# Kernel optimization log

Measured on AMD Instinct MI355X. Metric: run time of the kernel, lower is better.

Reference implementation:

```python
import jax, jax.numpy as jnp
import numpy as np

D_MODEL = 2048
NUM_HEADS = 32
NUM_KV_GROUPS = 8
D_K = D_MODEL // NUM_HEADS  # 64
KV_DIM = D_K * NUM_KV_GROUPS  # 512
B, S = 2, 2048


def setup_inputs() -> dict:
    key = jax.random.key(0)
    ks = jax.random.split(key, 9)
    sd = 1.0 / np.sqrt(D_MODEL).astype(np.float32)
    return {
        "x": jax.random.normal(ks[0], (B, S, D_MODEL), jnp.float32),
        "wq": jax.random.normal(ks[1], (D_MODEL, D_MODEL), jnp.float32) * sd,
        "bq": jnp.zeros((D_MODEL,), jnp.float32),
        "wk": jax.random.normal(ks[2], (D_MODEL, KV_DIM), jnp.float32) * sd,
        "bk": jnp.zeros((KV_DIM,), jnp.float32),
        "wv": jax.random.normal(ks[3], (D_MODEL, KV_DIM), jnp.float32) * sd,
        "bv": jnp.zeros((KV_DIM,), jnp.float32),
        "wo": jax.random.normal(ks[4], (D_MODEL, D_MODEL), jnp.float32) * sd,
        "bo": jnp.zeros((D_MODEL,), jnp.float32),
    }


def reference(x, wq, bq, wk, bk, wv, bv, wo, bo):
    b, s, _ = x.shape
    # projections (torch Linear = x @ W^T + b; weights here stored as (in,out))
    Q = (x @ wq + bq).reshape(b, s, NUM_HEADS, D_K).transpose(0, 2, 1, 3)       # [B,H,S,dk]
    K = (x @ wk + bk).reshape(b, s, NUM_KV_GROUPS, D_K).transpose(0, 2, 1, 3)   # [B,G,S,dk]
    V = (x @ wv + bv).reshape(b, s, NUM_KV_GROUPS, D_K).transpose(0, 2, 1, 3)   # [B,G,S,dk]
    kv_repeat = NUM_HEADS // NUM_KV_GROUPS
    K_rep = jnp.repeat(K, kv_repeat, axis=1)  # [B,H,S,dk]
    V_rep = jnp.repeat(V, kv_repeat, axis=1)  # [B,H,S,dk]
    scale = 1.0 / jnp.sqrt(jnp.asarray(D_K, x.dtype))
    attn_scores = jnp.einsum("bhqd,bhkd->bhqk", Q, K_rep) * scale
    attn_weights = jax.nn.softmax(attn_scores, axis=-1)                          # [B,H,S,S]
    context = jnp.einsum("bhqk,bhkd->bhqd", attn_weights, V_rep)
    context = context.transpose(0, 2, 1, 3).reshape(b, s, D_MODEL)
    return context @ wo + bo
```

## Files before the change

kernel.cpp:

```cpp
#include <hip/hip_runtime.h>
#include <hip/hip_bf16.h>

typedef __bf16 v8bf16 __attribute__((ext_vector_type(8)));
typedef __bf16 bf16x4 __attribute__((ext_vector_type(4)));
typedef float  f32x4  __attribute__((ext_vector_type(4)));

#define D_MODEL 2048
#define S_LEN   2048
#define NHEADS  32
#define NGROUPS 8
#define DK      64
#define NTOK    4096
#define NQKV    3072
#define QSCALE  0.18033688011112042f

__device__ __forceinline__ void lds_load16(const void* g, void* l) {
  __builtin_amdgcn_global_load_lds(
      (__attribute__((address_space(1))) unsigned int*)g,
      (__attribute__((address_space(3))) unsigned int*)l, 16, 0, 0);
}

__device__ __forceinline__ int sw64(int row, int col) {
  return row * 64 + (col ^ ((row & 7) << 3));
}

__global__ __launch_bounds__(256)
void cvt_f32_bf16(const float* __restrict__ in, __bf16* __restrict__ out, int n) {
  int i = (blockIdx.x * 256 + threadIdx.x) * 4;
  if (i >= n) return;
  float4 v = *(const float4*)(in + i);
  bf16x4 o = { (__bf16)v.x, (__bf16)v.y, (__bf16)v.z, (__bf16)v.w };
  *(bf16x4*)(out + i) = o;
}

__global__ __launch_bounds__(256)
void transpose_cvt(const float* __restrict__ in, __bf16* __restrict__ out, int R, int C) {
  __shared__ float tile[32][33];
  int tx = threadIdx.x, ty = threadIdx.y;
  int c0 = blockIdx.x * 32, r0 = blockIdx.y * 32;
#pragma unroll
  for (int j = 0; j < 4; j++)
    tile[ty + 8 * j][tx] = in[(size_t)(r0 + ty + 8 * j) * C + c0 + tx];
  __syncthreads();
#pragma unroll
  for (int j = 0; j < 4; j++)
    out[(size_t)(c0 + ty + 8 * j) * R + r0 + tx] = (__bf16)tile[tx][ty + 8 * j];
}

__global__ __launch_bounds__(256)
void transpose_bf16(const __bf16* __restrict__ in, __bf16* __restrict__ out,
                    int R, int C, int ldin, int ldout) {
  __shared__ __bf16 tile[32][33];
  int tx = threadIdx.x, ty = threadIdx.y;
  int c0 = blockIdx.x * 32, r0 = blockIdx.y * 32;
#pragma unroll
  for (int j = 0; j < 4; j++)
    tile[ty + 8 * j][tx] = in[(size_t)(r0 + ty + 8 * j) * ldin + c0 + tx];
  __syncthreads();
#pragma unroll
  for (int j = 0; j < 4; j++)
    out[(size_t)(c0 + ty + 8 * j) * ldout + r0 + tx] = tile[tx][ty + 8 * j];
}

template <int MODE, int BN>
__global__ __launch_bounds__(512, 1)
void gemm_big(const __bf16* __restrict__ A, const __bf16* __restrict__ BT,
              const float* __restrict__ b0, const float* __restrict__ b1,
              const float* __restrict__ b2,
              __bf16* __restrict__ Cb, float* __restrict__ Cf,
              int M, int N, int K) {
  constexpr int FN = BN / 64;
  __shared__ __bf16 Alds[2 * 256 * 64];
  __shared__ __bf16 Blds[2 * BN * 64];
  const int t = threadIdx.x;
  const int lane = t & 63, w = t >> 6;
  const int lr = lane & 15, lg = lane >> 4;
  const int wm = w >> 2, wn = w & 3;
  const int cpx = gridDim.x >> 3;
  const int swz = (blockIdx.x & 7) * cpx + (blockIdx.x >> 3);
  const int nbx = N / BN;
  const int m0 = (swz / nbx) * 256, n0 = (swz % nbx) * BN;
  const int scol = (((t & 7) ^ ((t >> 3) & 7)) << 3);

  const __bf16* ap = A + (size_t)(m0 + (t >> 3)) * K + scol;
  const __bf16* bp = BT + (size_t)(n0 + (t >> 3)) * K + scol;

  auto stage = [&](int buf) {
    __bf16* ad = Alds + buf * 16384 + t * 8;
    __bf16* bd = Blds + buf * BN * 64 + t * 8;
#pragma unroll
    for (int i = 0; i < 4; i++) lds_load16(ap + (size_t)i * 64 * K, ad + i * 4096);
#pragma unroll
    for (int i = 0; i < FN; i++) lds_load16(bp + (size_t)i * 64 * K, bd + i * 4096);
    ap += 64; bp += 64;
  };

  const f32x4 fz = {0.f, 0.f, 0.f, 0.f};
  f32x4 acc[8][FN];
#pragma unroll
  for (int fm = 0; fm < 8; fm++)
#pragma unroll
    for (int fn = 0; fn < FN; fn++) acc[fm][fn] = fz;

  auto compute = [&](int buf) {
    const __bf16* Ab = Alds + buf * 16384;
    const __bf16* Bb = Blds + buf * BN * 64;
#pragma unroll
    for (int ks = 0; ks < 2; ks++) {
      v8bf16 bfr[FN];
#pragma unroll
      for (int fn = 0; fn < FN; fn++)
        bfr[fn] = *(const v8bf16*)&Bb[sw64(wn * (BN / 4) + fn * 16 + lr, ks * 32 + lg * 8)];
      __builtin_amdgcn_s_setprio(1);
#pragma unroll
      for (int fm = 0; fm < 8; fm++) {
        v8bf16 af = *(const v8bf16*)&Ab[sw64(wm * 128 + fm * 16 + lr, ks * 32 + lg * 8)];
#pragma unroll
        for (int fn = 0; fn < FN; fn++)
          acc[fm][fn] = __builtin_amdgcn_mfma_f32_16x16x32_bf16(af, bfr[fn], acc[fm][fn], 0, 0, 0);
      }
      __builtin_amdgcn_s_setprio(0);
    }
  };

  stage(0);
  stage(1);
  for (int kt = 0; kt < 32; kt++) {
    if (kt < 31) {
      if constexpr (FN == 3) asm volatile("s_waitcnt vmcnt(7)" ::: "memory");
      else                   asm volatile("s_waitcnt vmcnt(6)" ::: "memory");
    } else {
      asm volatile("s_waitcnt vmcnt(0)" ::: "memory");
    }
    __builtin_amdgcn_s_barrier();
    __builtin_amdgcn_sched_barrier(0);
    compute(kt & 1);
    if (kt < 30) {
      __builtin_amdgcn_sched_barrier(0);
      __builtin_amdgcn_s_barrier();
      __builtin_amdgcn_sched_barrier(0);
      stage(kt & 1);
    }
  }

#pragma unroll
  for (int fn = 0; fn < FN; fn++) {
    int col = n0 + wn * (BN / 4) + fn * 16 + lr;
    float bias, scale = 1.0f;
    if (MODE == 0) {
      if (col < 2048)      { bias = b0[col];        scale = QSCALE; }
      else if (col < 2560) { bias = b1[col - 2048]; }
      else                 { bias = b2[col - 2560]; }
    } else {
      bias = b0[col];
    }
#pragma unroll
    for (int fm = 0; fm < 8; fm++)
#pragma unroll
      for (int r = 0; r < 4; r++) {
        int row = m0 + wm * 128 + fm * 16 + lg * 4 + r;
        float v = acc[fm][fn][r] + bias;
        if (MODE == 0) Cb[(size_t)row * N + col] = (__bf16)(v * scale);
        else           Cf[(size_t)row * N + col] = v;
      }
  }
}

__global__ __launch_bounds__(512, 2)
void attn_kernel(const __bf16* __restrict__ QKV, const __bf16* __restrict__ VT,
                 __bf16* __restrict__ ctx) {
  __shared__ __bf16 smem[26624];
  const int t = threadIdx.x;
  const int lane = t & 63, w = t >> 6;
  const int lr = lane & 15, lg = lane >> 4;
  const int flat = blockIdx.y * 8 + blockIdx.x;
  const int swz = (flat & 7) * 64 + (flat >> 3);
  const int qt = swz & 7, bh = swz >> 3;
  const int b = bh >> 5, h = bh & 31, g = h >> 2;
  const int q0 = qt * 256;
  const int scol = (((t & 7) ^ ((t >> 3) & 7)) << 3);

  v8bf16 qa[2][2];
#pragma unroll
  for (int mi = 0; mi < 2; mi++)
#pragma unroll
    for (int dk2 = 0; dk2 < 2; dk2++)
      qa[mi][dk2] = *(const v8bf16*)(QKV +
          (size_t)(b * S_LEN + q0 + w * 32 + mi * 16 + lr) * NQKV + h * DK + dk2 * 32 + lg * 8);

  const __bf16* kp = QKV + (size_t)(b * S_LEN + (t >> 3)) * NQKV + D_MODEL + g * DK + scol;
  const __bf16* vp = VT + (size_t)(g * DK + (t >> 3)) * NTOK + b * S_LEN + scol;

  lds_load16(kp, smem + t * 8);
  lds_load16(vp, smem + 4096 + t * 8);
  __syncthreads();

  const int kloff0 = lr * 64 + ((lg * 8) ^ ((lr & 7) << 3));
  const int kloff1 = lr * 64 + ((32 + lg * 8) ^ ((lr & 7) << 3));
  __bf16* Pw = smem + 16384 + w * 1280;

  const __bf16 one1 = (__bf16)1.0f;
  const v8bf16 ones = { one1, one1, one1, one1, one1, one1, one1, one1 };
  const f32x4 fz = {0.f, 0.f, 0.f, 0.f};
  f32x4 o[2][4], o_sum[2];
  o_sum[0] = fz; o_sum[1] = fz;
#pragma unroll
  for (int mi = 0; mi < 2; mi++)
#pragma unroll
    for (int nd = 0; nd < 4; nd++) o[mi][nd] = fz;

#pragma unroll 2
  for (int kt = 0; kt < 32; kt++) {
    if (kt < 31) {
      __bf16* nb = smem + ((kt & 1) ^ 1) * 8192;
      lds_load16(kp + (size_t)64 * NQKV, nb + t * 8);
      lds_load16(vp + 64, nb + 4096 + t * 8);
      kp += (size_t)64 * NQKV;
      vp += 64;
    }
    const __bf16* Kb = smem + (kt & 1) * 8192;
    const __bf16* k0 = Kb + kloff0;
    const __bf16* k1 = Kb + kloff1;

    f32x4 st[4][2];
#pragma unroll
    for (int ni = 0; ni < 4; ni++) { st[ni][0] = fz; st[ni][1] = fz; }
    __builtin_amdgcn_s_setprio(1);
#pragma unroll
    for (int ni = 0; ni < 4; ni++) {
      v8bf16 kb = *(const v8bf16*)(k0 + ni * 1024);
      st[ni][0] = __builtin_amdgcn_mfma_f32_16x16x32_bf16(kb, qa[0][0], st[ni][0], 0, 0, 0);
      st[ni][1] = __builtin_amdgcn_mfma_f32_16x16x32_bf16(kb, qa[1][0], st[ni][1], 0, 0, 0);
    }
#pragma unroll
    for (int ni = 0; ni < 4; ni++) {
      v8bf16 kb = *(const v8bf16*)(k1 + ni * 1024);
      st[ni][0] = __builtin_amdgcn_mfma_f32_16x16x32_bf16(kb, qa[0][1], st[ni][0], 0, 0, 0);
      st[ni][1] = __builtin_amdgcn_mfma_f32_16x16x32_bf16(kb, qa[1][1], st[ni][1], 0, 0, 0);
    }
    __builtin_amdgcn_s_setprio(0);

#pragma unroll
    for (int ks = 0; ks < 2; ks++) {
      const __bf16* vbase = (ks ? k1 : k0) + 4096;
#pragma unroll
      for (int mi = 0; mi < 2; mi++)
#pragma unroll
        for (int ni2 = 0; ni2 < 2; ni2++) {
          f32x4 sv = st[2 * ks + ni2][mi];
          bf16x4 pk = { (__bf16)exp2f(sv[0]), (__bf16)exp2f(sv[1]),
                        (__bf16)exp2f(sv[2]), (__bf16)exp2f(sv[3]) };
          *(bf16x4*)(Pw + (mi * 16 + lr) * 40 + ni2 * 16 + lg * 4) = pk;
        }
      v8bf16 pa0 = *(const v8bf16*)(Pw + lr * 40 + lg * 8);
      v8bf16 pa1 = *(const v8bf16*)(Pw + (16 + lr) * 40 + lg * 8);
      __builtin_amdgcn_s_setprio(1);
#pragma unroll
      for (int nd = 0; nd < 4; nd++) {
        v8bf16 vb = *(const v8bf16*)(vbase + nd * 1024);
        o[0][nd] = __builtin_amdgcn_mfma_f32_16x16x32_bf16(pa0, vb, o[0][nd], 0, 0, 0);
        o[1][nd] = __builtin_amdgcn_mfma_f32_16x16x32_bf16(pa1, vb, o[1][nd], 0, 0, 0);
      }
      o_sum[0] = __builtin_amdgcn_mfma_f32_16x16x32_bf16(pa0, ones, o_sum[0], 0, 0, 0);
      o_sum[1] = __builtin_amdgcn_mfma_f32_16x16x32_bf16(pa1, ones, o_sum[1], 0, 0, 0);
      __builtin_amdgcn_s_setprio(0);
    }

    __syncthreads();
  }

#pragma unroll
  for (int mi = 0; mi < 2; mi++)
#pragma unroll
    for (int r = 0; r < 4; r++) {
      float inv = 1.0f / o_sum[mi][r];
      int row = b * S_LEN + q0 + w * 32 + mi * 16 + lg * 4 + r;
#pragma unroll
      for (int nd = 0; nd < 4; nd++)
        ctx[(size_t)row * D_MODEL + h * DK + nd * 16 + lr] = (__bf16)(o[mi][nd][r] * inv);
    }
}

extern "C" void kernel_launch(void* const* d_in, const int* in_sizes, int n_in,
                              void* d_out, int out_size, void* d_ws, size_t ws_size,
                              hipStream_t stream) {
  (void)in_sizes; (void)n_in; (void)out_size; (void)ws_size;
  const float* x  = (const float*)d_in[0];
  const float* wq = (const float*)d_in[1];
  const float* bq = (const float*)d_in[2];
  const float* wk = (const float*)d_in[3];
  const float* bk = (const float*)d_in[4];
  const float* wv = (const float*)d_in[5];
  const float* bv = (const float*)d_in[6];
  const float* wo = (const float*)d_in[7];
  const float* bo = (const float*)d_in[8];

  char* ws = (char*)d_ws;
  __bf16* xb    = (__bf16*)(ws);
  __bf16* wqkvT = (__bf16*)(ws + 16777216);
  __bf16* woT   = (__bf16*)(ws + 29360128);
  __bf16* QKVb  = (__bf16*)(ws + 37748736);
  __bf16* VbT   = (__bf16*)(ws + 62914560);
  __bf16* ctx   = (__bf16*)(ws + 67108864);

  dim3 tb(32, 8);
  cvt_f32_bf16<<<8192, 256, 0, stream>>>(x, xb, NTOK * D_MODEL);
  transpose_cvt<<<dim3(64, 64), tb, 0, stream>>>(wq, wqkvT, 2048, 2048);
  transpose_cvt<<<dim3(16, 64), tb, 0, stream>>>(wk, wqkvT + 2048 * 2048, 2048, 512);
  transpose_cvt<<<dim3(16, 64), tb, 0, stream>>>(wv, wqkvT + 2560 * 2048, 2048, 512);
  transpose_cvt<<<dim3(64, 64), tb, 0, stream>>>(wo, woT, 2048, 2048);

  gemm_big<0, 192><<<dim3(256), 512, 0, stream>>>(xb, wqkvT, bq, bk, bv,
                                                  QKVb, nullptr, NTOK, NQKV, 2048);
  transpose_bf16<<<dim3(16, 128), tb, 0, stream>>>(QKVb + 2560, VbT, 4096, 512, 3072, 4096);
  attn_kernel<<<dim3(8, 64), 512, 0, stream>>>(QKVb, VbT, ctx);
  gemm_big<1, 128><<<dim3(256), 512, 0, stream>>>(ctx, woT, bo, nullptr, nullptr,
                                                  nullptr, (float*)d_out, NTOK, 2048, 2048);
}
```

Before: 231.1 us.

## Interleave chunked A/B global-to-LDS loads with MFMA phases using triple-buffered B

The GEMM main loop is split into four compute phases, each handling half of the M fragments and half of K. Global-to-LDS loads for the next one or two K tiles are spread across those phases instead of being issued as one block after compute. B moves to a triple buffer so tile kt+2 can be prefetched early. A stays double-buffered, with row chunks refilled as soon as they are consumed. The aim is to overlap memory traffic with MFMA work more evenly, at the cost of more barriers per iteration and more LDS use.

```diff
diff --git a/kernel.cpp b/kernel.cpp
--- a/kernel.cpp
+++ b/kernel.cpp
@@ -71,7 +71,7 @@
               int M, int N, int K) {
   constexpr int FN = BN / 64;
   __shared__ __bf16 Alds[2 * 256 * 64];
-  __shared__ __bf16 Blds[2 * BN * 64];
+  __shared__ __bf16 Blds[3 * BN * 64];
   const int t = threadIdx.x;
   const int lane = t & 63, w = t >> 6;
   const int lr = lane & 15, lg = lane >> 4;
@@ -82,17 +82,16 @@
   const int m0 = (swz / nbx) * 256, n0 = (swz % nbx) * BN;
   const int scol = (((t & 7) ^ ((t >> 3) & 7)) << 3);
 
-  const __bf16* ap = A + (size_t)(m0 + (t >> 3)) * K + scol;
-  const __bf16* bp = BT + (size_t)(n0 + (t >> 3)) * K + scol;
-
-  auto stage = [&](int buf) {
-    __bf16* ad = Alds + buf * 16384 + t * 8;
-    __bf16* bd = Blds + buf * BN * 64 + t * 8;
-#pragma unroll
-    for (int i = 0; i < 4; i++) lds_load16(ap + (size_t)i * 64 * K, ad + i * 4096);
-#pragma unroll
-    for (int i = 0; i < FN; i++) lds_load16(bp + (size_t)i * 64 * K, bd + i * 4096);
-    ap += 64; bp += 64;
+  const __bf16* Abase = A + (size_t)(m0 + (t >> 3)) * K + scol;
+  const __bf16* Bbase = BT + (size_t)(n0 + (t >> 3)) * K + scol;
+
+  auto stageA = [&](int tile, int c) {
+    lds_load16(Abase + (size_t)(c * 64) * K + tile * 64,
+               Alds + (tile & 1) * 16384 + c * 4096 + t * 8);
+  };
+  auto stageB = [&](int tile, int bi, int c) {
+    lds_load16(Bbase + (size_t)(c * 64) * K + tile * 64,
+               Blds + bi * (BN * 64) + c * 4096 + t * 8);
   };
 
   const f32x4 fz = {0.f, 0.f, 0.f, 0.f};
@@ -102,45 +101,113 @@
 #pragma unroll
     for (int fn = 0; fn < FN; fn++) acc[fm][fn] = fz;
 
-  auto compute = [&](int buf) {
-    const __bf16* Ab = Alds + buf * 16384;
-    const __bf16* Bb = Blds + buf * BN * 64;
-#pragma unroll
-    for (int ks = 0; ks < 2; ks++) {
-      v8bf16 bfr[FN];
-#pragma unroll
-      for (int fn = 0; fn < FN; fn++)
-        bfr[fn] = *(const v8bf16*)&Bb[sw64(wn * (BN / 4) + fn * 16 + lr, ks * 32 + lg * 8)];
-      __builtin_amdgcn_s_setprio(1);
-#pragma unroll
-      for (int fm = 0; fm < 8; fm++) {
-        v8bf16 af = *(const v8bf16*)&Ab[sw64(wm * 128 + fm * 16 + lr, ks * 32 + lg * 8)];
-#pragma unroll
-        for (int fn = 0; fn < FN; fn++)
-          acc[fm][fn] = __builtin_amdgcn_mfma_f32_16x16x32_bf16(af, bfr[fn], acc[fm][fn], 0, 0, 0);
-      }
-      __builtin_amdgcn_s_setprio(0);
-    }
-  };
-
-  stage(0);
-  stage(1);
+#pragma unroll
+  for (int c = 0; c < 4; c++) stageA(0, c);
+#pragma unroll
+  for (int c = 0; c < FN; c++) stageB(0, 0, c);
+  stageA(1, 0);
+  stageA(1, 2);
+#pragma unroll
+  for (int c = 0; c < FN; c++) stageB(1, 1, c);
+
+  int bcur = 0, bn1 = 1, bn2 = 2;
   for (int kt = 0; kt < 32; kt++) {
     if (kt < 31) {
-      if constexpr (FN == 3) asm volatile("s_waitcnt vmcnt(7)" ::: "memory");
-      else                   asm volatile("s_waitcnt vmcnt(6)" ::: "memory");
+      if constexpr (FN == 3) asm volatile("s_waitcnt vmcnt(5)" ::: "memory");
+      else                   asm volatile("s_waitcnt vmcnt(4)" ::: "memory");
     } else {
       asm volatile("s_waitcnt vmcnt(0)" ::: "memory");
     }
     __builtin_amdgcn_s_barrier();
     __builtin_amdgcn_sched_barrier(0);
-    compute(kt & 1);
-    if (kt < 30) {
-      __builtin_amdgcn_sched_barrier(0);
-      __builtin_amdgcn_s_barrier();
-      __builtin_amdgcn_sched_barrier(0);
-      stage(kt & 1);
-    }
+
+    const __bf16* Ab = Alds + (kt & 1) * 16384;
+    const __bf16* Bb = Blds + bcur * (BN * 64);
+    v8bf16 bfr[2][FN];
+
+    {
+#pragma unroll
+      for (int fn = 0; fn < FN; fn++)
+        bfr[0][fn] = *(const v8bf16*)&Bb[sw64(wn * (BN / 4) + fn * 16 + lr, lg * 8)];
+      v8bf16 af[4];
+#pragma unroll
+      for (int j = 0; j < 4; j++)
+        af[j] = *(const v8bf16*)&Ab[sw64(wm * 128 + j * 16 + lr, lg * 8)];
+      if (kt < 31) stageA(kt + 1, 1);
+      __builtin_amdgcn_s_barrier();
+      __builtin_amdgcn_sched_barrier(0);
+      __builtin_amdgcn_s_setprio(1);
+#pragma unroll
+      for (int j = 0; j < 4; j++)
+#pragma unroll
+        for (int fn = 0; fn < FN; fn++)
+          acc[j][fn] = __builtin_amdgcn_mfma_f32_16x16x32_bf16(af[j], bfr[0][fn], acc[j][fn], 0, 0, 0);
+      __builtin_amdgcn_s_setprio(0);
+      __builtin_amdgcn_sched_barrier(0);
+      __builtin_amdgcn_s_barrier();
+    }
+    {
+#pragma unroll
+      for (int fn = 0; fn < FN; fn++)
+        bfr[1][fn] = *(const v8bf16*)&Bb[sw64(wn * (BN / 4) + fn * 16 + lr, 32 + lg * 8)];
+      v8bf16 af[4];
+#pragma unroll
+      for (int j = 0; j < 4; j++)
+        af[j] = *(const v8bf16*)&Ab[sw64(wm * 128 + j * 16 + lr, 32 + lg * 8)];
+      if (kt < 31) stageA(kt + 1, 3);
+      __builtin_amdgcn_s_barrier();
+      __builtin_amdgcn_sched_barrier(0);
+      __builtin_amdgcn_s_setprio(1);
+#pragma unroll
+      for (int j = 0; j < 4; j++)
+#pragma unroll
+        for (int fn = 0; fn < FN; fn++)
+          acc[j][fn] = __builtin_amdgcn_mfma_f32_16x16x32_bf16(af[j], bfr[1][fn], acc[j][fn], 0, 0, 0);
+      __builtin_amdgcn_s_setprio(0);
+      __builtin_amdgcn_sched_barrier(0);
+      __builtin_amdgcn_s_barrier();
+    }
+    {
+      v8bf16 af[4];
+#pragma unroll
+      for (int j = 0; j < 4; j++)
+        af[j] = *(const v8bf16*)&Ab[sw64(wm * 128 + 64 + j * 16 + lr, lg * 8)];
+      if (kt < 30) { stageA(kt + 2, 0); stageB(kt + 2, bn2, 0); }
+      __builtin_amdgcn_s_barrier();
+      __builtin_amdgcn_sched_barrier(0);
+      __builtin_amdgcn_s_setprio(1);
+#pragma unroll
+      for (int j = 0; j < 4; j++)
+#pragma unroll
+        for (int fn = 0; fn < FN; fn++)
+          acc[4 + j][fn] = __builtin_amdgcn_mfma_f32_16x16x32_bf16(af[j], bfr[0][fn], acc[4 + j][fn], 0, 0, 0);
+      __builtin_amdgcn_s_setprio(0);
+      __builtin_amdgcn_sched_barrier(0);
+      __builtin_amdgcn_s_barrier();
+    }
+    {
+      v8bf16 af[4];
+#pragma unroll
+      for (int j = 0; j < 4; j++)
+        af[j] = *(const v8bf16*)&Ab[sw64(wm * 128 + 64 + j * 16 + lr, 32 + lg * 8)];
+      if (kt < 30) {
+        stageA(kt + 2, 2);
+        stageB(kt + 2, bn2, 1);
+        if constexpr (FN == 3) stageB(kt + 2, bn2, 2);
+      }
+      __builtin_amdgcn_s_barrier();
+      __builtin_amdgcn_sched_barrier(0);
+      __builtin_amdgcn_s_setprio(1);
+#pragma unroll
+      for (int j = 0; j < 4; j++)
+#pragma unroll
+        for (int fn = 0; fn < FN; fn++)
+          acc[4 + j][fn] = __builtin_amdgcn_mfma_f32_16x16x32_bf16(af[j], bfr[1][fn], acc[4 + j][fn], 0, 0, 0);
+      __builtin_amdgcn_s_setprio(0);
+      __builtin_amdgcn_sched_barrier(0);
+    }
+
+    int tmp = bcur; bcur = bn1; bn1 = bn2; bn2 = tmp;
   }
 
 #pragma unroll
```

Result: faster. 223.2 us (-3.4%).
